# Kernel optimization log

Measured on AMD Instinct MI355X. Metric: run time of the kernel, lower is better.

## Reference

```python
import jax, jax.numpy as jnp
import numpy as np

STRIDE = 1
PAD = 3  # kernel_size // 2 = 7 // 2


def setup_inputs() -> dict:
    key = jax.random.key(0)
    k1, k2, k3 = jax.random.split(key, 3)
    B, Cin, T = 32, 128, 4096
    K, Cout, ks = 4, 256, 7
    x = jax.random.normal(k1, (B, Cin, T), dtype=jnp.float32)
    weight = jax.random.normal(k2, (K, Cout, Cin, ks), dtype=jnp.float32) * 0.01
    bias = jnp.zeros((K, Cout), dtype=jnp.float32)
    rw = jax.random.normal(k3, (K, Cin), dtype=jnp.float32) * 0.05
    rb = jnp.zeros((K,), dtype=jnp.float32)
    return {"x": x, "weight": weight, "bias": bias, "rw": rw, "rb": rb}


def reference(x, weight, bias, rw, rb):
    # x: [B, Cin, T]; weight: [K, Cout, Cin, ks]; bias: [K, Cout]
    K, Cout, Cin, ks = weight.shape
    B = x.shape[0]
    # routing: adaptive avg pool over T -> Linear -> softmax
    pooled = jnp.mean(x, axis=-1)                      # [B, Cin]
    alpha = jax.nn.softmax(pooled @ rw.T + rb, axis=-1)  # [B, K]
    # all K conv branches in one conv by folding K into out-channels
    w_all = weight.reshape(K * Cout, Cin, ks)
    y = jax.lax.conv_general_dilated(
        x, w_all, window_strides=(STRIDE,), padding=[(PAD, PAD)],
        dimension_numbers=("NCH", "OIH", "NCH"))      # [B, K*Cout, T']
    Tp = y.shape[-1]
    y = y.reshape(B, K, Cout, Tp) + bias[None, :, :, None]
    # softmax-routed weighted sum over the K branches
    out = jnp.einsum("bk,bkct->bct", alpha, y)         # [B, Cout, T']
    return out
```

## Files before the change

### kernel.cpp

```cpp
#include <hip/hip_runtime.h>
#include <stdint.h>


#define TP 4102

#define XT_OFF     0u
#define WEFF_OFF   33603584u
#define POOLED_OFF 48283648u
#define BEFF_OFF   48300032u

typedef short short8 __attribute__((ext_vector_type(8)));
typedef float f32x4 __attribute__((ext_vector_type(4)));

__device__ __forceinline__ unsigned short f2bf(float f) {
  unsigned int u = __builtin_bit_cast(unsigned int, f);
  u += 0x7fffu + ((u >> 16) & 1u);
  return (unsigned short)(u >> 16);
}

__global__ __launch_bounds__(256) void k_transpose_pool(
    const float* __restrict__ x, unsigned short* __restrict__ xt,
    float* __restrict__ pooled) {
  __shared__ __align__(16) unsigned short xs[128 * 136];
  __shared__ float pbuf[128 * 33];
  int blk = blockIdx.x;
  int b = blk >> 5, tc = blk & 31;
  int t0 = tc << 7;
  int tid = threadIdx.x;
  int lane32 = tid & 31, grp8 = tid >> 5;

  #pragma unroll
  for (int i = 0; i < 16; ++i) {
    int ci = i * 8 + grp8;
    const float4 v = *(const float4*)(x + (size_t)(b * 128 + ci) * 4096 + t0 + lane32 * 4);
    unsigned short h0 = f2bf(v.x), h1 = f2bf(v.y), h2 = f2bf(v.z), h3 = f2bf(v.w);
    uint2 pk;
    pk.x = (unsigned)h0 | ((unsigned)h1 << 16);
    pk.y = (unsigned)h2 | ((unsigned)h3 << 16);
    *(uint2*)(&xs[ci * 136 + lane32 * 4]) = pk;
    pbuf[ci * 33 + lane32] = v.x + v.y + v.z + v.w;
  }
  __syncthreads();
  if (tid < 128) {
    float s = 0.f;
    #pragma unroll
    for (int l = 0; l < 32; ++l) s += pbuf[tid * 33 + l];
    atomicAdd(&pooled[b * 128 + tid], s);
  }
  #pragma unroll
  for (int it = 0; it < 8; ++it) {
    int idx = it * 256 + tid;
    int tr = idx & 127, g = idx >> 7;
    unsigned short h[8];
    #pragma unroll
    for (int u = 0; u < 8; ++u) h[u] = xs[(g * 8 + u) * 136 + tr];
    uint4 o;
    o.x = (unsigned)h[0] | ((unsigned)h[1] << 16);
    o.y = (unsigned)h[2] | ((unsigned)h[3] << 16);
    o.z = (unsigned)h[4] | ((unsigned)h[5] << 16);
    o.w = (unsigned)h[6] | ((unsigned)h[7] << 16);
    *(uint4*)(xt + ((size_t)(b * 16 + g) * TP + 3 + t0 + tr) * 8) = o;
  }
  uint4 z; z.x = z.y = z.z = z.w = 0;
  if (tc == 0 && tid < 64) {
    int g = tid >> 2, pr = tid & 3;
    if (pr < 3) *(uint4*)(xt + ((size_t)(b * 16 + g) * TP + pr) * 8) = z;
  }
  if (tc == 31 && tid < 64) {
    int g = tid >> 2, pr = tid & 3;
    if (pr < 3) *(uint4*)(xt + ((size_t)(b * 16 + g) * TP + 4099 + pr) * 8) = z;
  }
}

__global__ __launch_bounds__(256) void k_fold(
    const float* __restrict__ w, const float* __restrict__ pooled,
    const float* __restrict__ rw, const float* __restrict__ rb,
    const float* __restrict__ bias, unsigned short* __restrict__ weff,
    float* __restrict__ bias_eff) {
  __shared__ float al[32][4];
  int tid = threadIdx.x;
  if (tid < 128) {
    int b = tid >> 2, k = tid & 3;
    const float* pp = pooled + b * 128;
    const float* rwk = rw + k * 128;
    float s = rb[k];
    #pragma unroll 8
    for (int j = 0; j < 128; ++j) s += pp[j] * (1.0f / 4096.0f) * rwk[j];
    al[b][k] = s;
  }
  __syncthreads();
  if (tid < 32) {
    float l0 = al[tid][0], l1 = al[tid][1], l2 = al[tid][2], l3 = al[tid][3];
    float m = fmaxf(fmaxf(l0, l1), fmaxf(l2, l3));
    float e0 = __expf(l0 - m), e1 = __expf(l1 - m);
    float e2 = __expf(l2 - m), e3 = __expf(l3 - m);
    float inv = 1.0f / (e0 + e1 + e2 + e3);
    al[tid][0] = e0 * inv; al[tid][1] = e1 * inv;
    al[tid][2] = e2 * inv; al[tid][3] = e3 * inv;
  }
  __syncthreads();
  if (blockIdx.x == 0) {
    #pragma unroll
    for (int b = 0; b < 32; ++b) {
      float s = 0.f;
      #pragma unroll
      for (int k = 0; k < 4; ++k) s += al[b][k] * bias[k * 256 + tid];
      bias_eff[b * 256 + tid] = s;
    }
  }
  int gid = blockIdx.x * 256 + tid;
  int cb = gid / 14336;
  int r = gid - cb * 14336;
  int step = r >> 9;
  int cblk = (r >> 6) & 7;
  int lpos = r & 63;
  int q = lpos >> 4, n16 = lpos & 15;
  int kk = step & 1, half = (step >> 1) & 1, s7 = step >> 2;
  int cout = cb * 128 + cblk * 16 + n16;
  int ci0 = half * 64 + (kk * 4 + q) * 8;
  float wv[4][8];
  #pragma unroll
  for (int k = 0; k < 4; ++k) {
    const float* src = w + ((size_t)(k * 256 + cout) * 128 + ci0) * 7 + s7;
    #pragma unroll
    for (int j = 0; j < 8; ++j) wv[k][j] = src[j * 7];
  }
  unsigned short* dst =
      weff + (((size_t)(cb * 28 + step) * 8 + cblk) * 64 + lpos) * 8;
  #pragma unroll 4
  for (int b = 0; b < 32; ++b) {
    float a0 = al[b][0], a1 = al[b][1], a2 = al[b][2], a3 = al[b][3];
    unsigned short h[8];
    #pragma unroll
    for (int j = 0; j < 8; ++j)
      h[j] = f2bf(a0 * wv[0][j] + a1 * wv[1][j] + a2 * wv[2][j] + a3 * wv[3][j]);
    uint4 o;
    o.x = (unsigned)h[0] | ((unsigned)h[1] << 16);
    o.y = (unsigned)h[2] | ((unsigned)h[3] << 16);
    o.z = (unsigned)h[4] | ((unsigned)h[5] << 16);
    o.w = (unsigned)h[6] | ((unsigned)h[7] << 16);
    *(uint4*)(dst + (size_t)b * 229376) = o;
  }
}

__global__ __launch_bounds__(256, 2) void k_conv(
    const unsigned short* __restrict__ xt, const unsigned short* __restrict__ weff,
    const float* __restrict__ bias_eff, float* __restrict__ out) {
  __shared__ __align__(16) unsigned short xs[16 * 262 * 8];
  int blk = blockIdx.x;
  int b = blk >> 5, cb = (blk >> 4) & 1, tb = blk & 15;
  int bcb = b * 2 + cb;
  int tid = threadIdx.x;
  int wave = tid >> 6, lane = tid & 63;
  int q = lane >> 4, n16 = lane & 15;
  int wm = wave & 1, wn = wave >> 1;
  int t00 = tb << 8;

  const unsigned short* xtb = xt + (size_t)b * 16 * TP * 8;
  #pragma unroll
  for (int g = 0; g < 16; ++g) {
    *(uint4*)(&xs[((size_t)g * 262 + tid) * 8]) =
        *(const uint4*)(xtb + ((size_t)g * TP + t00 + tid) * 8);
  }
  if (tid < 128) {
    int g = tid >> 3, r8 = tid & 7;
    if (r8 < 6) {
      int row = 256 + r8;
      *(uint4*)(&xs[((size_t)g * 262 + row) * 8]) =
          *(const uint4*)(xtb + ((size_t)g * TP + t00 + row) * 8);
    }
  }
  __syncthreads();

  f32x4 acc[4][8];
  #pragma unroll
  for (int mi = 0; mi < 4; ++mi)
    #pragma unroll
    for (int ni = 0; ni < 8; ++ni)
      acc[mi][ni] = (f32x4){0.f, 0.f, 0.f, 0.f};

  const short8* wfrag = (const short8*)weff + (size_t)bcb * 14336 + (wm * 4) * 64 + lane;

  short8 av[4];
  #pragma unroll
  for (int mi = 0; mi < 4; ++mi) av[mi] = wfrag[mi * 64];

  #pragma unroll 2
  for (int step = 0; step < 28; ++step) {
    int s = step >> 2, half = (step >> 1) & 1, kk = step & 1;
    short8 avn[4];
    if (step < 27) {
      #pragma unroll
      for (int mi = 0; mi < 4; ++mi)
        avn[mi] = wfrag[(step + 1) * 512 + mi * 64];
    }
    short8 bv[8];
    int prow = (half * 8 + kk * 4 + q) * 262 + s;
    #pragma unroll
    for (int ni = 0; ni < 8; ++ni) {
      int tt = wn * 128 + ni * 16 + n16;
      bv[ni] = *(const short8*)(&xs[(size_t)(prow + tt) * 8]);
    }
    #pragma unroll
    for (int mi = 0; mi < 4; ++mi)
      #pragma unroll
      for (int ni = 0; ni < 8; ++ni)
        acc[mi][ni] = __builtin_amdgcn_mfma_f32_16x16x32_bf16(
            av[mi], bv[ni], acc[mi][ni], 0, 0, 0);
    #pragma unroll
    for (int mi = 0; mi < 4; ++mi) av[mi] = avn[mi];
  }

  int crow0 = b * 256 + cb * 128;
  #pragma unroll
  for (int mi = 0; mi < 4; ++mi) {
    #pragma unroll
    for (int r = 0; r < 4; ++r) {
      int c = wm * 64 + mi * 16 + q * 4 + r;
      float bb = bias_eff[crow0 + c];
      float* orow = out + (size_t)(crow0 + c) * 4096 + t00;
      #pragma unroll
      for (int ni = 0; ni < 8; ++ni)
        orow[wn * 128 + ni * 16 + n16] = acc[mi][ni][r] + bb;
    }
  }
}

extern "C" void kernel_launch(void* const* d_in, const int* in_sizes, int n_in,
                              void* d_out, int out_size, void* d_ws, size_t ws_size,
                              hipStream_t stream) {
  const float* x    = (const float*)d_in[0];
  const float* w    = (const float*)d_in[1];
  const float* bias = (const float*)d_in[2];
  const float* rw   = (const float*)d_in[3];
  const float* rb   = (const float*)d_in[4];
  float* out = (float*)d_out;
  char* ws = (char*)d_ws;
  unsigned short* xt   = (unsigned short*)(ws + XT_OFF);
  unsigned short* weff = (unsigned short*)(ws + WEFF_OFF);
  float* pooled        = (float*)(ws + POOLED_OFF);
  float* bias_eff      = (float*)(ws + BEFF_OFF);

  hipMemsetAsync(pooled, 0, 32 * 128 * sizeof(float), stream);
  hipLaunchKernelGGL(k_transpose_pool, dim3(1024), dim3(256), 0, stream, x, xt, pooled);
  hipLaunchKernelGGL(k_fold, dim3(112), dim3(256), 0, stream,
                     w, pooled, rw, rb, bias, weff, bias_eff);
  hipLaunchKernelGGL(k_conv, dim3(1024), dim3(256), 0, stream, xt, weff, bias_eff, out);
}
```

Measured before the change: 249.6 us.

## Fuse bf16 transpose into conv load, loop both channel blocks per tile

Drops the separate transpose kernel and its bf16 intermediate buffer. The conv kernel now reads fp32 x directly, converts it to bf16 and transposes it into shared memory with zero padding at the edges. Each block handles both 128-channel halves, so the staged x tile is reused across all 256 outputs. Pooling moves to a per-row reduction kernel with no atomics or memset, and the block index is swizzled. The fp32 reads in the conv stage are strided by channel (8 rows 16KB apart per thread), which may coalesce worse. Half as many blocks may also leave the MFMA stage less parallel.

```diff
diff --git a/kernel.cpp b/kernel.cpp
--- a/kernel.cpp
+++ b/kernel.cpp
@@ -2,12 +2,9 @@
 #include <stdint.h>
 
 
-#define TP 4102
-
-#define XT_OFF     0u
-#define WEFF_OFF   33603584u
-#define POOLED_OFF 48283648u
-#define BEFF_OFF   48300032u
+#define WEFF_OFF   0u
+#define POOLED_OFF 14680064u
+#define BEFF_OFF   14696448u
 
 typedef short short8 __attribute__((ext_vector_type(8)));
 typedef float f32x4 __attribute__((ext_vector_type(4)));
@@ -18,58 +15,23 @@
   return (unsigned short)(u >> 16);
 }
 
-__global__ __launch_bounds__(256) void k_transpose_pool(
-    const float* __restrict__ x, unsigned short* __restrict__ xt,
-    float* __restrict__ pooled) {
-  __shared__ __align__(16) unsigned short xs[128 * 136];
-  __shared__ float pbuf[128 * 33];
-  int blk = blockIdx.x;
-  int b = blk >> 5, tc = blk & 31;
-  int t0 = tc << 7;
-  int tid = threadIdx.x;
-  int lane32 = tid & 31, grp8 = tid >> 5;
-
+__global__ __launch_bounds__(256) void k_pool(const float* __restrict__ x,
+                                              float* __restrict__ pooled) {
+  __shared__ float ws4[4];
+  int row = blockIdx.x;
+  const float* src = x + (size_t)row * 4096 + threadIdx.x * 16;
+  float s = 0.f;
   #pragma unroll
-  for (int i = 0; i < 16; ++i) {
-    int ci = i * 8 + grp8;
-    const float4 v = *(const float4*)(x + (size_t)(b * 128 + ci) * 4096 + t0 + lane32 * 4);
-    unsigned short h0 = f2bf(v.x), h1 = f2bf(v.y), h2 = f2bf(v.z), h3 = f2bf(v.w);
-    uint2 pk;
-    pk.x = (unsigned)h0 | ((unsigned)h1 << 16);
-    pk.y = (unsigned)h2 | ((unsigned)h3 << 16);
-    *(uint2*)(&xs[ci * 136 + lane32 * 4]) = pk;
-    pbuf[ci * 33 + lane32] = v.x + v.y + v.z + v.w;
-  }
-  __syncthreads();
-  if (tid < 128) {
-    float s = 0.f;
-    #pragma unroll
-    for (int l = 0; l < 32; ++l) s += pbuf[tid * 33 + l];
-    atomicAdd(&pooled[b * 128 + tid], s);
+  for (int i = 0; i < 4; ++i) {
+    float4 v = *(const float4*)(src + i * 4);
+    s += (v.x + v.y) + (v.z + v.w);
   }
   #pragma unroll
-  for (int it = 0; it < 8; ++it) {
-    int idx = it * 256 + tid;
-    int tr = idx & 127, g = idx >> 7;
-    unsigned short h[8];
-    #pragma unroll
-    for (int u = 0; u < 8; ++u) h[u] = xs[(g * 8 + u) * 136 + tr];
-    uint4 o;
-    o.x = (unsigned)h[0] | ((unsigned)h[1] << 16);
-    o.y = (unsigned)h[2] | ((unsigned)h[3] << 16);
-    o.z = (unsigned)h[4] | ((unsigned)h[5] << 16);
-    o.w = (unsigned)h[6] | ((unsigned)h[7] << 16);
-    *(uint4*)(xt + ((size_t)(b * 16 + g) * TP + 3 + t0 + tr) * 8) = o;
-  }
-  uint4 z; z.x = z.y = z.z = z.w = 0;
-  if (tc == 0 && tid < 64) {
-    int g = tid >> 2, pr = tid & 3;
-    if (pr < 3) *(uint4*)(xt + ((size_t)(b * 16 + g) * TP + pr) * 8) = z;
-  }
-  if (tc == 31 && tid < 64) {
-    int g = tid >> 2, pr = tid & 3;
-    if (pr < 3) *(uint4*)(xt + ((size_t)(b * 16 + g) * TP + 4099 + pr) * 8) = z;
-  }
+  for (int off = 32; off > 0; off >>= 1) s += __shfl_down(s, off);
+  int lane = threadIdx.x & 63, wv = threadIdx.x >> 6;
+  if (lane == 0) ws4[wv] = s;
+  __syncthreads();
+  if (threadIdx.x == 0) pooled[row] = (ws4[0] + ws4[1]) + (ws4[2] + ws4[3]);
 }
 
 __global__ __launch_bounds__(256) void k_fold(
@@ -143,85 +105,110 @@
   }
 }
 
-__global__ __launch_bounds__(256, 2) void k_conv(
-    const unsigned short* __restrict__ xt, const unsigned short* __restrict__ weff,
+__global__ __launch_bounds__(256, 2) void k_conv2(
+    const float* __restrict__ x, const unsigned short* __restrict__ weff,
     const float* __restrict__ bias_eff, float* __restrict__ out) {
   __shared__ __align__(16) unsigned short xs[16 * 262 * 8];
-  int blk = blockIdx.x;
-  int b = blk >> 5, cb = (blk >> 4) & 1, tb = blk & 15;
-  int bcb = b * 2 + cb;
+  int phys = blockIdx.x;
+  int logical = (phys & 7) * 64 + (phys >> 3);
+  int b = logical >> 4, tb = logical & 15;
   int tid = threadIdx.x;
+  int t00 = tb << 8;
+
+  {
+    const float* xbase = x + (size_t)b * 128 * 4096;
+    int xrow = t00 - 3 + tid;
+    bool valid = (unsigned)xrow < 4096u;
+    #pragma unroll
+    for (int g = 0; g < 16; ++g) {
+      float f[8];
+      #pragma unroll
+      for (int u = 0; u < 8; ++u)
+        f[u] = valid ? xbase[(size_t)(g * 8 + u) * 4096 + xrow] : 0.f;
+      uint4 o;
+      o.x = (unsigned)f2bf(f[0]) | ((unsigned)f2bf(f[1]) << 16);
+      o.y = (unsigned)f2bf(f[2]) | ((unsigned)f2bf(f[3]) << 16);
+      o.z = (unsigned)f2bf(f[4]) | ((unsigned)f2bf(f[5]) << 16);
+      o.w = (unsigned)f2bf(f[6]) | ((unsigned)f2bf(f[7]) << 16);
+      *(uint4*)(&xs[(g * 262 + tid) * 8]) = o;
+    }
+    if (tid < 128) {
+      int g = tid >> 3, r8 = tid & 7;
+      if (r8 < 6) {
+        int row2 = 256 + r8;
+        int xrow2 = t00 - 3 + row2;
+        bool v2 = (unsigned)xrow2 < 4096u;
+        float f[8];
+        #pragma unroll
+        for (int u = 0; u < 8; ++u)
+          f[u] = v2 ? xbase[(size_t)(g * 8 + u) * 4096 + xrow2] : 0.f;
+        uint4 o;
+        o.x = (unsigned)f2bf(f[0]) | ((unsigned)f2bf(f[1]) << 16);
+        o.y = (unsigned)f2bf(f[2]) | ((unsigned)f2bf(f[3]) << 16);
+        o.z = (unsigned)f2bf(f[4]) | ((unsigned)f2bf(f[5]) << 16);
+        o.w = (unsigned)f2bf(f[6]) | ((unsigned)f2bf(f[7]) << 16);
+        *(uint4*)(&xs[(g * 262 + row2) * 8]) = o;
+      }
+    }
+  }
+  __syncthreads();
+
   int wave = tid >> 6, lane = tid & 63;
   int q = lane >> 4, n16 = lane & 15;
   int wm = wave & 1, wn = wave >> 1;
-  int t00 = tb << 8;
-
-  const unsigned short* xtb = xt + (size_t)b * 16 * TP * 8;
-  #pragma unroll
-  for (int g = 0; g < 16; ++g) {
-    *(uint4*)(&xs[((size_t)g * 262 + tid) * 8]) =
-        *(const uint4*)(xtb + ((size_t)g * TP + t00 + tid) * 8);
-  }
-  if (tid < 128) {
-    int g = tid >> 3, r8 = tid & 7;
-    if (r8 < 6) {
-      int row = 256 + r8;
-      *(uint4*)(&xs[((size_t)g * 262 + row) * 8]) =
-          *(const uint4*)(xtb + ((size_t)g * TP + t00 + row) * 8);
-    }
-  }
-  __syncthreads();
-
-  f32x4 acc[4][8];
-  #pragma unroll
-  for (int mi = 0; mi < 4; ++mi)
-    #pragma unroll
-    for (int ni = 0; ni < 8; ++ni)
-      acc[mi][ni] = (f32x4){0.f, 0.f, 0.f, 0.f};
-
-  const short8* wfrag = (const short8*)weff + (size_t)bcb * 14336 + (wm * 4) * 64 + lane;
-
-  short8 av[4];
-  #pragma unroll
-  for (int mi = 0; mi < 4; ++mi) av[mi] = wfrag[mi * 64];
-
-  #pragma unroll 2
-  for (int step = 0; step < 28; ++step) {
-    int s = step >> 2, half = (step >> 1) & 1, kk = step & 1;
-    short8 avn[4];
-    if (step < 27) {
+  const short8* wb8 = (const short8*)weff + (size_t)b * 28672;
+
+  for (int cb = 0; cb < 2; ++cb) {
+    f32x4 acc[4][8];
+    #pragma unroll
+    for (int mi = 0; mi < 4; ++mi)
+      #pragma unroll
+      for (int ni = 0; ni < 8; ++ni)
+        acc[mi][ni] = (f32x4){0.f, 0.f, 0.f, 0.f};
+
+    const short8* wfrag = wb8 + (cb * 224 + wm * 4) * 64 + lane;
+    short8 av[4];
+    #pragma unroll
+    for (int mi = 0; mi < 4; ++mi) av[mi] = wfrag[mi * 64];
+
+    #pragma unroll 2
+    for (int step = 0; step < 28; ++step) {
+      int s = step >> 2, half = (step >> 1) & 1, kk = step & 1;
+      short8 avn[4];
+      if (step < 27) {
+        #pragma unroll
+        for (int mi = 0; mi < 4; ++mi)
+          avn[mi] = wfrag[(step + 1) * 512 + mi * 64];
+      }
+      short8 bv[8];
+      int prow = (half * 8 + kk * 4 + q) * 262 + s;
+      #pragma unroll
+      for (int ni = 0; ni < 8; ++ni) {
+        int tt = wn * 128 + ni * 16 + n16;
+        bv[ni] = *(const short8*)(&xs[(size_t)(prow + tt) * 8]);
+      }
       #pragma unroll
       for (int mi = 0; mi < 4; ++mi)
-        avn[mi] = wfrag[(step + 1) * 512 + mi * 64];
-    }
-    short8 bv[8];
-    int prow = (half * 8 + kk * 4 + q) * 262 + s;
-    #pragma unroll
-    for (int ni = 0; ni < 8; ++ni) {
-      int tt = wn * 128 + ni * 16 + n16;
-      bv[ni] = *(const short8*)(&xs[(size_t)(prow + tt) * 8]);
-    }
-    #pragma unroll
-    for (int mi = 0; mi < 4; ++mi)
-      #pragma unroll
-      for (int ni = 0; ni < 8; ++ni)
-        acc[mi][ni] = __builtin_amdgcn_mfma_f32_16x16x32_bf16(
-            av[mi], bv[ni], acc[mi][ni], 0, 0, 0);
-    #pragma unroll
-    for (int mi = 0; mi < 4; ++mi) av[mi] = avn[mi];
-  }
-
-  int crow0 = b * 256 + cb * 128;
-  #pragma unroll
-  for (int mi = 0; mi < 4; ++mi) {
-    #pragma unroll
-    for (int r = 0; r < 4; ++r) {
-      int c = wm * 64 + mi * 16 + q * 4 + r;
-      float bb = bias_eff[crow0 + c];
-      float* orow = out + (size_t)(crow0 + c) * 4096 + t00;
-      #pragma unroll
-      for (int ni = 0; ni < 8; ++ni)
-        orow[wn * 128 + ni * 16 + n16] = acc[mi][ni][r] + bb;
+        #pragma unroll
+        for (int ni = 0; ni < 8; ++ni)
+          acc[mi][ni] = __builtin_amdgcn_mfma_f32_16x16x32_bf16(
+              av[mi], bv[ni], acc[mi][ni], 0, 0, 0);
+      #pragma unroll
+      for (int mi = 0; mi < 4; ++mi) av[mi] = avn[mi];
+    }
+
+    int crow0 = b * 256 + cb * 128;
+    #pragma unroll
+    for (int mi = 0; mi < 4; ++mi) {
+      #pragma unroll
+      for (int r = 0; r < 4; ++r) {
+        int c = wm * 64 + mi * 16 + q * 4 + r;
+        float bb = bias_eff[crow0 + c];
+        float* orow = out + (size_t)(crow0 + c) * 4096 + t00;
+        #pragma unroll
+        for (int ni = 0; ni < 8; ++ni)
+          orow[wn * 128 + ni * 16 + n16] = acc[mi][ni][r] + bb;
+      }
     }
   }
 }
@@ -236,14 +223,13 @@
   const float* rb   = (const float*)d_in[4];
   float* out = (float*)d_out;
   char* ws = (char*)d_ws;
-  unsigned short* xt   = (unsigned short*)(ws + XT_OFF);
   unsigned short* weff = (unsigned short*)(ws + WEFF_OFF);
   float* pooled        = (float*)(ws + POOLED_OFF);
   float* bias_eff      = (float*)(ws + BEFF_OFF);
 
-  hipMemsetAsync(pooled, 0, 32 * 128 * sizeof(float), stream);
-  hipLaunchKernelGGL(k_transpose_pool, dim3(1024), dim3(256), 0, stream, x, xt, pooled);
-  hipLaunchKernelGGL(k_fold, dim3(112), dim3(256), 0, stream,
+  hipLaunchKernelGGL(k_pool,  dim3(4096), dim3(256), 0, stream, x, pooled);
+  hipLaunchKernelGGL(k_fold,  dim3(112),  dim3(256), 0, stream,
                      w, pooled, rw, rb, bias, weff, bias_eff);
-  hipLaunchKernelGGL(k_conv, dim3(1024), dim3(256), 0, stream, xt, weff, bias_eff, out);
-}
+  hipLaunchKernelGGL(k_conv2, dim3(512),  dim3(256), 0, stream,
+                     x, weff, bias_eff, out);
+}
```

Result: faster. 239.2 us (-4.2%).
